# Kernel tuning notes

Measured on AMD Instinct MI355X. Metric: run time of the kernel, lower is better.

The kernel has to match this reference:

```python
import jax, jax.numpy as jnp
import numpy as np

HEADS = 16
DIM_HEAD = 64


def setup_inputs() -> dict:
    key = jax.random.key(0)
    k1, k2, k3 = jax.random.split(key, 3)
    b, n, dim = 8, 4096, 1024
    inner = HEADS * DIM_HEAD  # 1024
    x = jax.random.normal(k1, (b, n, dim), dtype=jnp.float32)
    # torch Linear stored transposed; here W_qkv is [in, out] so y = x @ W_qkv
    W_qkv = jax.random.normal(k2, (dim, 4 * inner), dtype=jnp.float32) * (dim ** -0.5)
    W_out = jax.random.normal(k3, (inner, dim), dtype=jnp.float32) * (inner ** -0.5)
    b_out = jnp.zeros((dim,), dtype=jnp.float32)
    return {"x": x, "W_qkv": W_qkv, "W_out": W_out, "b_out": b_out}


def reference(x, W_qkv, W_out, b_out):
    b, n, dim = x.shape
    h, d = HEADS, DIM_HEAD
    scale = d ** -0.5
    qkv = x @ W_qkv  # [b, n, 4*h*d]
    q, k, v, v2 = jnp.split(qkv, 4, axis=-1)
    # rearrange 'b n (h d) -> b h n d'
    to_heads = lambda t: t.reshape(b, n, h, d).transpose(0, 2, 1, 3)
    q, k, v, v2 = map(to_heads, (q, k, v, v2))
    # channel-wise attention: dots = q^T @ k over the sequence axis -> [b,h,d,d]
    dots = jnp.einsum('bhnd,bhne->bhde', q, k) * scale
    attn = jax.nn.softmax(dots, axis=-1)
    # v^T @ v2 -> [b,h,d,d]
    vv = jnp.einsum('bhnd,bhne->bhde', v, v2)
    out = jnp.einsum('bhde,bhef->bhdf', attn, vv)  # [b,h,d,d]
    # rearrange 'b h n d -> b n (h d)' with n == dim_head here
    out = out.transpose(0, 2, 1, 3).reshape(b, d, h * d)  # [b, dim_head, inner]
    return out @ W_out + b_out  # [b, dim_head, dim]
```

## Files before the change

kernel.cpp:

```cpp
#include <hip/hip_runtime.h>
#include <hip/hip_bf16.h>
#include <stdint.h>

typedef _Float16 f16;
typedef _Float16 f16x8 __attribute__((ext_vector_type(8)));
typedef float f32x4 __attribute__((ext_vector_type(4)));

#define AS1 __attribute__((address_space(1)))
#define AS3 __attribute__((address_space(3)))

__global__ __launch_bounds__(256) void tr_cvt_all(
    const float* __restrict__ x, const float* __restrict__ Wqkv,
    const float* __restrict__ Wout,
    f16* __restrict__ xT, f16* __restrict__ WqkvT, f16* __restrict__ WoutT)
{
    __shared__ float tile[64][65];
    const int id = blockIdx.x;
    const int t = threadIdx.x;

    const float* src; f16* dst; int R, C, c0, r0;
    if (id < 8192) {
        const int b = id >> 10, rem = id & 1023;
        src = x + (size_t)b * 4096 * 1024;
        dst = xT + (size_t)b * 4096 * 1024;
        R = 4096; C = 1024;
        c0 = (rem & 15) * 64; r0 = (rem >> 4) * 64;
    } else if (id < 9216) {
        const int rem = id - 8192;
        src = Wqkv; dst = WqkvT;
        R = 1024; C = 4096;
        c0 = (rem & 63) * 64; r0 = (rem >> 6) * 64;
    } else {
        const int rem = id - 9216;
        src = Wout; dst = WoutT;
        R = 1024; C = 1024;
        c0 = (rem & 15) * 64; r0 = (rem >> 4) * 64;
    }

    {
        const int cc = (t & 15) * 4;
        const int rr = t >> 4;
#pragma unroll
        for (int p = 0; p < 4; ++p) {
            const int r = rr + p * 16;
            const float4 v = *(const float4*)(src + (size_t)(r0 + r) * C + c0 + cc);
            tile[r][cc + 0] = v.x; tile[r][cc + 1] = v.y;
            tile[r][cc + 2] = v.z; tile[r][cc + 3] = v.w;
        }
    }
    __syncthreads();
    {
        const int rq = (t & 15) * 4;
        const int cp = t >> 4;
#pragma unroll
        for (int p = 0; p < 4; ++p) {
            const int c = cp + p * 16;
            ushort4 o;
            f16 h0 = (f16)tile[rq + 0][c];
            f16 h1 = (f16)tile[rq + 1][c];
            f16 h2 = (f16)tile[rq + 2][c];
            f16 h3 = (f16)tile[rq + 3][c];
            o.x = __builtin_bit_cast(unsigned short, h0);
            o.y = __builtin_bit_cast(unsigned short, h1);
            o.z = __builtin_bit_cast(unsigned short, h2);
            o.w = __builtin_bit_cast(unsigned short, h3);
            *(ushort4*)(dst + (size_t)(c0 + c) * R + r0 + rq) = o;
        }
    }
}

__device__ __forceinline__ void stage256(
    const f16* __restrict__ src, int ld, char* ldsbase, int tid)
{
    const int lane = tid & 63;
    const int gch = ((lane & 7) ^ (lane >> 3)) * 8;
    const int rowl = tid >> 3;
    const int wbase = (tid >> 3) & ~7;
#pragma unroll
    for (int p = 0; p < 4; ++p) {
        const f16* s = src + (size_t)(p * 64 + rowl) * ld + gch;
        __builtin_amdgcn_global_load_lds(
            (const AS1 uint32_t*)s,
            (AS3 uint32_t*)(ldsbase + (p * 64 + wbase) * 128), 16, 0, 0);
    }
}

__device__ __forceinline__ void gemm256_core(
    const f16* __restrict__ A, const f16* __restrict__ Bt,
    int lda, int ldb, int nsteps,
    f16* As, f16* Bs, f32x4 (&acc)[8][4], int tid)
{
    const int lane = tid & 63, w = tid >> 6;
    const int wr = w >> 2, wc = w & 3;
    const int cl = lane & 15, kg = lane >> 4, b7 = lane & 7;

    stage256(A, lda, (char*)As, tid);
    stage256(Bt, ldb, (char*)Bs, tid);

#pragma unroll 1
    for (int t = 0; t < nsteps; ++t) {
        const int cur = t & 1;
        if (t + 1 < nsteps) {
            const int k0 = (t + 1) * 64;
            stage256(A + k0, lda, (char*)As + (cur ^ 1) * 32768, tid);
            stage256(Bt + k0, ldb, (char*)Bs + (cur ^ 1) * 32768, tid);
            asm volatile("s_waitcnt vmcnt(8)" ::: "memory");
        } else {
            asm volatile("s_waitcnt vmcnt(0)" ::: "memory");
        }
        __builtin_amdgcn_s_barrier();
        const f16* Ab = As + cur * 16384;
        const f16* Bb = Bs + cur * 16384;
#pragma unroll
        for (int kk = 0; kk < 2; ++kk) {
            const int ch = (kk * 4 + kg) ^ b7;
            f16x8 af[8], bf[4];
#pragma unroll
            for (int i = 0; i < 8; ++i)
                af[i] = *(const f16x8*)&Ab[(wr * 128 + i * 16 + cl) * 64 + ch * 8];
#pragma unroll
            for (int j = 0; j < 4; ++j)
                bf[j] = *(const f16x8*)&Bb[(wc * 64 + j * 16 + cl) * 64 + ch * 8];
#pragma unroll
            for (int i = 0; i < 8; ++i)
#pragma unroll
                for (int j = 0; j < 4; ++j)
                    acc[i][j] = __builtin_amdgcn_mfma_f32_16x16x32_f16(af[i], bf[j], acc[i][j], 0, 0, 0);
        }
        __builtin_amdgcn_s_barrier();
    }
}

__global__ __launch_bounds__(512, 2) void gemm_syk256(
    const f16* __restrict__ xT, f16* __restrict__ Gp)
{
    __shared__ f16 As[2 * 256 * 64];
    __shared__ f16 Bs[2 * 256 * 64];
    const int orig = blockIdx.x;
    const int l = (orig & 7) * 32 + (orig >> 3);
    const int tile = l & 15, b = (l >> 4) & 7, s = l >> 7;
    const int ti = tile >> 2, tj = tile & 3;

    const f16* base = xT + (size_t)b * (1024 * 4096) + (size_t)s * 2048;
    const f16* A  = base + (size_t)ti * 256 * 4096;
    const f16* Bt = base + (size_t)tj * 256 * 4096;

    f32x4 acc[8][4];
#pragma unroll
    for (int i = 0; i < 8; ++i)
#pragma unroll
        for (int j = 0; j < 4; ++j) acc[i][j] = f32x4{0.f, 0.f, 0.f, 0.f};

    gemm256_core(A, Bt, 4096, 4096, 32, As, Bs, acc, threadIdx.x);

    f16* out = Gp + ((size_t)s * 8 + b) * 1048576;
    const int lane = threadIdx.x & 63, w = threadIdx.x >> 6;
    const int wr = w >> 2, wc = w & 3;
    const int cl = lane & 15, rg = lane >> 4;
#pragma unroll
    for (int i = 0; i < 8; ++i)
#pragma unroll
        for (int j = 0; j < 4; ++j)
#pragma unroll
            for (int q = 0; q < 4; ++q) {
                const int row = ti * 256 + wr * 128 + i * 16 + rg * 4 + q;
                const int col = tj * 256 + wc * 64 + j * 16 + cl;
                out[(size_t)row * 1024 + col] = (f16)acc[i][j][q];
            }
}

__global__ __launch_bounds__(256) void reduce_sum(
    const f16* __restrict__ Gp, f16* __restrict__ G)
{
    const size_t i = ((size_t)blockIdx.x * 256 + threadIdx.x) * 8;
    const f16x8 a = *(const f16x8*)(Gp + i);
    const f16x8 c = *(const f16x8*)(Gp + 8388608 + i);
    f16x8 o;
#pragma unroll
    for (int j = 0; j < 8; ++j) o[j] = (f16)((float)a[j] + (float)c[j]);
    *(f16x8*)(G + i) = o;
}

__global__ __launch_bounds__(512, 2) void gemm_qv256(
    const f16* __restrict__ WqkvT, const f16* __restrict__ G,
    f16* __restrict__ UW2)
{
    __shared__ f16 As[2 * 256 * 64];
    __shared__ f16 Bs[2 * 256 * 64];
    const int orig = blockIdx.x;
    const int l = (orig & 7) * 32 + (orig >> 3);
    const int bx = l & 3, by = (l >> 2) & 7, b = l >> 5;
    const int arow = (by < 4) ? by * 256 : 2048 + (by - 4) * 256;

    const f16* A  = WqkvT + (size_t)arow * 1024;
    const f16* Bt = G + (size_t)b * 1048576 + (size_t)bx * 256 * 1024;

    f32x4 acc[8][4];
#pragma unroll
    for (int i = 0; i < 8; ++i)
#pragma unroll
        for (int j = 0; j < 4; ++j) acc[i][j] = f32x4{0.f, 0.f, 0.f, 0.f};

    gemm256_core(A, Bt, 1024, 1024, 16, As, Bs, acc, threadIdx.x);

    f16* C = UW2 + (size_t)b * 2097152;
    const int lane = threadIdx.x & 63, w = threadIdx.x >> 6;
    const int wr = w >> 2, wc = w & 3;
    const int cl = lane & 15, rg = lane >> 4;
#pragma unroll
    for (int i = 0; i < 8; ++i)
#pragma unroll
        for (int j = 0; j < 4; ++j) {
            const int cc = bx * 256 + wc * 64 + j * 16 + cl;
#pragma unroll
            for (int q = 0; q < 4; ++q) {
                const int rr = by * 256 + wr * 128 + i * 16 + rg * 4 + q;
                C[(size_t)rr * 1024 + cc] = (f16)acc[i][j][q];
            }
        }
}

__device__ __forceinline__ void gemm_body(
    const f16* __restrict__ A, const f16* __restrict__ Bt,
    int lda, int ldb, int K, f16* As, f16* Bs,
    f32x4 (&acc)[4][4], int tid)
{
    const int lane = tid & 63, w = tid >> 6;
    const int wr = w >> 1, wc = w & 1;
    const int lrow = lane >> 3;
    const int lcol = (lane & 7) * 8;
    for (int k0 = 0; k0 < K; k0 += 64) {
#pragma unroll
        for (int p = 0; p < 4; ++p) {
            const f16* sa = A + (size_t)(p * 32 + w * 8 + lrow) * lda + k0 + lcol;
            __builtin_amdgcn_global_load_lds(
                (const AS1 uint32_t*)sa,
                (AS3 uint32_t*)((char*)As + p * 4096 + w * 1024), 16, 0, 0);
            const f16* sb = Bt + (size_t)(p * 32 + w * 8 + lrow) * ldb + k0 + lcol;
            __builtin_amdgcn_global_load_lds(
                (const AS1 uint32_t*)sb,
                (AS3 uint32_t*)((char*)Bs + p * 4096 + w * 1024), 16, 0, 0);
        }
        __syncthreads();
#pragma unroll
        for (int kk = 0; kk < 2; ++kk) {
            f16x8 af[4], bfr[4];
#pragma unroll
            for (int i = 0; i < 4; ++i)
                af[i] = *(const f16x8*)&As[(wr * 64 + i * 16 + (lane & 15)) * 64 + kk * 32 + (lane >> 4) * 8];
#pragma unroll
            for (int j = 0; j < 4; ++j)
                bfr[j] = *(const f16x8*)&Bs[(wc * 64 + j * 16 + (lane & 15)) * 64 + kk * 32 + (lane >> 4) * 8];
#pragma unroll
            for (int i = 0; i < 4; ++i)
#pragma unroll
                for (int j = 0; j < 4; ++j)
                    acc[i][j] = __builtin_amdgcn_mfma_f32_16x16x32_f16(af[i], bfr[j], acc[i][j], 0, 0, 0);
        }
        __syncthreads();
    }
}

__global__ __launch_bounds__(256) void gemm_out(
    const f16* __restrict__ A, const f16* __restrict__ Bt,
    const float* __restrict__ bias, float* __restrict__ Cout)
{
    __shared__ f16 As[128 * 64];
    __shared__ f16 Bs[128 * 64];
    const int tn0 = blockIdx.x * 128;
    const int tm0 = blockIdx.y * 128;
    f32x4 acc[4][4];
#pragma unroll
    for (int i = 0; i < 4; ++i)
#pragma unroll
        for (int j = 0; j < 4; ++j) acc[i][j] = f32x4{0.f, 0.f, 0.f, 0.f};

    gemm_body(A + (size_t)tm0 * 1024, Bt + (size_t)tn0 * 1024,
              1024, 1024, 1024, As, Bs, acc, threadIdx.x);

    const int lane = threadIdx.x & 63, w = threadIdx.x >> 6;
    const int wr = w >> 1, wc = w & 1;
    const int cl = lane & 15, rg = lane >> 4;
#pragma unroll
    for (int i = 0; i < 4; ++i)
#pragma unroll
        for (int j = 0; j < 4; ++j) {
            const int cc = tn0 + wc * 64 + j * 16 + cl;
            const float bv = bias[cc];
#pragma unroll
            for (int q = 0; q < 4; ++q) {
                const int rr = tm0 + wr * 64 + i * 16 + rg * 4 + q;
                Cout[(size_t)rr * 1024 + cc] = acc[i][j][q] + bv;
            }
        }
}

__global__ __launch_bounds__(512) void attn_small(
    const f16* __restrict__ UW2, const f16* __restrict__ WqkvT,
    f16* __restrict__ O)
{
    __shared__ float dots[64][66];
    __shared__ float vv[64][66];
    const int h = blockIdx.x, b = blockIdx.y;
    const int tid = threadIdx.x, lane = tid & 63, w = tid >> 6;
    const int isVV = w >> 2;
    const int kq = w & 3;

    const f16* Arows = UW2 + (size_t)b * (2048 * 1024)
                           + (size_t)isVV * (1024 * 1024) + (size_t)h * 64 * 1024;
    const f16* Brows = WqkvT + (size_t)(isVV ? 3072 : 1024) * 1024 + (size_t)h * 64 * 1024;

    f32x4 acc[4][4];
#pragma unroll
    for (int i = 0; i < 4; ++i)
#pragma unroll
        for (int j = 0; j < 4; ++j) acc[i][j] = f32x4{0.f, 0.f, 0.f, 0.f};

    const int cl = lane & 15, kg = lane >> 4;
    for (int ks = 0; ks < 8; ++ks) {
        const int k0 = kq * 256 + ks * 32 + kg * 8;
        f16x8 af[4], bfr[4];
#pragma unroll
        for (int i = 0; i < 4; ++i)
            af[i] = *(const f16x8*)(Arows + (size_t)(i * 16 + cl) * 1024 + k0);
#pragma unroll
        for (int j = 0; j < 4; ++j)
            bfr[j] = *(const f16x8*)(Brows + (size_t)(j * 16 + cl) * 1024 + k0);
#pragma unroll
        for (int i = 0; i < 4; ++i)
#pragma unroll
            for (int j = 0; j < 4; ++j)
                acc[i][j] = __builtin_amdgcn_mfma_f32_16x16x32_f16(af[i], bfr[j], acc[i][j], 0, 0, 0);
    }

    float (*dst)[66] = isVV ? vv : dots;
#pragma unroll
    for (int r = 0; r < 4; ++r) {
        if (kq == r) {
            if (r == 0) {
#pragma unroll
                for (int i = 0; i < 4; ++i)
#pragma unroll
                    for (int j = 0; j < 4; ++j)
#pragma unroll
                        for (int q = 0; q < 4; ++q)
                            dst[i * 16 + kg * 4 + q][j * 16 + cl] = acc[i][j][q];
            } else {
#pragma unroll
                for (int i = 0; i < 4; ++i)
#pragma unroll
                    for (int j = 0; j < 4; ++j)
#pragma unroll
                        for (int q = 0; q < 4; ++q)
                            dst[i * 16 + kg * 4 + q][j * 16 + cl] += acc[i][j][q];
            }
        }
        __syncthreads();
    }

    if (tid < 64) {
        const int r = tid;
        float mx = -1e30f;
        for (int e = 0; e < 64; ++e) {
            const float v = dots[r][e] * 0.125f;
            dots[r][e] = v;
            mx = fmaxf(mx, v);
        }
        float s = 0.f;
        for (int e = 0; e < 64; ++e) {
            const float v = __expf(dots[r][e] - mx);
            dots[r][e] = v;
            s += v;
        }
        const float inv = 1.f / s;
        for (int e = 0; e < 64; ++e) dots[r][e] *= inv;
    }
    __syncthreads();

    {
        const int r = tid >> 3, f0 = (tid & 7) * 8;
        float o[8];
#pragma unroll
        for (int i = 0; i < 8; ++i) o[i] = 0.f;
        for (int e = 0; e < 64; ++e) {
            const float a = dots[r][e];
#pragma unroll
            for (int i = 0; i < 8; ++i) o[i] += a * vv[e][f0 + i];
        }
        f16* Od = O + (size_t)b * 64 * 1024 + (size_t)r * 1024 + h * 64 + f0;
#pragma unroll
        for (int i = 0; i < 8; ++i) Od[i] = (f16)o[i];
    }
}

extern "C" void kernel_launch(void* const* d_in, const int* in_sizes, int n_in,
                              void* d_out, int out_size, void* d_ws, size_t ws_size,
                              hipStream_t stream)
{
    const float* x    = (const float*)d_in[0];
    const float* Wqkv = (const float*)d_in[1];
    const float* Wout = (const float*)d_in[2];
    const float* bout = (const float*)d_in[3];

    char* ws = (char*)d_ws;
    f16* xT    = (f16*)(ws + 0);
    f16* WqkvT = (f16*)(ws + 67108864);
    f16* WoutT = (f16*)(ws + 75497472);
    f16* G     = (f16*)(ws + 77594624);
    f16* Gp    = (f16*)(ws + 94371840);
    f16* UW2   = (f16*)(ws + 94371840);
    f16* O     = (f16*)(ws + 127926272);

    tr_cvt_all<<<9472, 256, 0, stream>>>(x, Wqkv, Wout, xT, WqkvT, WoutT);

    gemm_syk256<<<256, 512, 0, stream>>>(xT, Gp);
    reduce_sum<<<4096, 256, 0, stream>>>(Gp, G);
    gemm_qv256<<<256, 512, 0, stream>>>(WqkvT, G, UW2);
    attn_small<<<dim3(16, 8), 512, 0, stream>>>(UW2, WqkvT, O);
    gemm_out<<<dim3(8, 4), 256, 0, stream>>>(O, WoutT, bout, (float*)d_out);
}
```

Before: 197.2 us.

## Exploit Gram-matrix symmetry: compute upper-triangle tiles only and mirror in reduce

The X^T X Gram GEMM now computes only the 10 upper-triangular 256x256 tiles per batch instead of all 16. The K dimension is rebalanced into three splits (22/21/21 steps) so that 240 blocks fit one wave. A new reduce kernel sums the three partials, writes each tile, and writes the transposed copy through shared memory for off-diagonal tiles. This cuts matrix-multiply work by roughly a third, at the cost of an extra partial, a transpose with possible LDS bank conflicts, and a large shared-memory footprint in the reduce.

Result: faster. 180.1 us (-8.7%).

```diff
diff --git a/kernel.cpp b/kernel.cpp
--- a/kernel.cpp
+++ b/kernel.cpp
@@ -137,11 +137,17 @@
     __shared__ f16 As[2 * 256 * 64];
     __shared__ f16 Bs[2 * 256 * 64];
     const int orig = blockIdx.x;
-    const int l = (orig & 7) * 32 + (orig >> 3);
-    const int tile = l & 15, b = (l >> 4) & 7, s = l >> 7;
-    const int ti = tile >> 2, tj = tile & 3;
-
-    const f16* base = xT + (size_t)b * (1024 * 4096) + (size_t)s * 2048;
+    const int l = (orig & 7) * 30 + (orig >> 3);
+    const int u = l % 10;
+    const int b = (l / 10) & 7;
+    const int s = l / 80;
+    int ti = 0, rem = u;
+    while (rem >= 4 - ti) { rem -= 4 - ti; ++ti; }
+    const int tj = ti + rem;
+    const int koff = (s == 0) ? 0 : (1408 + (s - 1) * 1344);
+    const int nst  = (s == 0) ? 22 : 21;
+
+    const f16* base = xT + (size_t)b * (1024 * 4096) + koff;
     const f16* A  = base + (size_t)ti * 256 * 4096;
     const f16* Bt = base + (size_t)tj * 256 * 4096;
 
@@ -151,9 +157,9 @@
 #pragma unroll
         for (int j = 0; j < 4; ++j) acc[i][j] = f32x4{0.f, 0.f, 0.f, 0.f};
 
-    gemm256_core(A, Bt, 4096, 4096, 32, As, Bs, acc, threadIdx.x);
-
-    f16* out = Gp + ((size_t)s * 8 + b) * 1048576;
+    gemm256_core(A, Bt, 4096, 4096, nst, As, Bs, acc, threadIdx.x);
+
+    f16* out = Gp + ((size_t)s * 80 + b * 10 + u) * 65536;
     const int lane = threadIdx.x & 63, w = threadIdx.x >> 6;
     const int wr = w >> 2, wc = w & 3;
     const int cl = lane & 15, rg = lane >> 4;
@@ -163,22 +169,62 @@
         for (int j = 0; j < 4; ++j)
 #pragma unroll
             for (int q = 0; q < 4; ++q) {
-                const int row = ti * 256 + wr * 128 + i * 16 + rg * 4 + q;
-                const int col = tj * 256 + wc * 64 + j * 16 + cl;
-                out[(size_t)row * 1024 + col] = (f16)acc[i][j][q];
+                const int row = wr * 128 + i * 16 + rg * 4 + q;
+                const int col = wc * 64 + j * 16 + cl;
+                out[row * 256 + col] = (f16)acc[i][j][q];
             }
 }
 
-__global__ __launch_bounds__(256) void reduce_sum(
+__global__ __launch_bounds__(256) void reduce_mirror(
     const f16* __restrict__ Gp, f16* __restrict__ G)
 {
-    const size_t i = ((size_t)blockIdx.x * 256 + threadIdx.x) * 8;
-    const f16x8 a = *(const f16x8*)(Gp + i);
-    const f16x8 c = *(const f16x8*)(Gp + 8388608 + i);
-    f16x8 o;
-#pragma unroll
-    for (int j = 0; j < 8; ++j) o[j] = (f16)((float)a[j] + (float)c[j]);
-    *(f16x8*)(G + i) = o;
+    __shared__ float tile[128][129];
+    const int q = blockIdx.x, u = blockIdx.y, b = blockIdx.z;
+    int ti = 0, rem = u;
+    while (rem >= 4 - ti) { rem -= 4 - ti; ++ti; }
+    const int tj = ti + rem;
+    const int qr = q >> 1, qc = q & 1;
+    const size_t tb = ((size_t)b * 10 + u) * 65536;
+    const size_t sstride = (size_t)80 * 65536;
+    f16* Gb = G + (size_t)b * 1048576;
+    const int t = threadIdx.x;
+
+#pragma unroll
+    for (int i = 0; i < 8; ++i) {
+        const int e = (i * 256 + t) * 8;
+        const int r = e >> 7, c = e & 127;
+        const size_t src = tb + (size_t)(qr * 128 + r) * 256 + qc * 128 + c;
+        float sum[8];
+#pragma unroll
+        for (int j = 0; j < 8; ++j) sum[j] = 0.f;
+#pragma unroll
+        for (int sp = 0; sp < 3; ++sp) {
+            const f16x8 v = *(const f16x8*)(Gp + sp * sstride + src);
+#pragma unroll
+            for (int j = 0; j < 8; ++j) sum[j] += (float)v[j];
+        }
+        f16x8 o;
+#pragma unroll
+        for (int j = 0; j < 8; ++j) {
+            o[j] = (f16)sum[j];
+            tile[r][c + j] = sum[j];
+        }
+        *(f16x8*)(Gb + (size_t)(ti * 256 + qr * 128 + r) * 1024
+                     + tj * 256 + qc * 128 + c) = o;
+    }
+    if (ti != tj) {
+        __syncthreads();
+#pragma unroll
+        for (int i = 0; i < 8; ++i) {
+            const int e = (i * 256 + t) * 8;
+            const int R = e >> 7, C = e & 127;
+            f16x8 o;
+#pragma unroll
+            for (int j = 0; j < 8; ++j) o[j] = (f16)tile[C + j][R];
+            *(f16x8*)(Gb + (size_t)(tj * 256 + qc * 128 + R) * 1024
+                         + ti * 256 + qr * 128 + C) = o;
+        }
+    }
 }
 
 __global__ __launch_bounds__(512, 2) void gemm_qv256(
@@ -413,8 +459,8 @@
 
     tr_cvt_all<<<9472, 256, 0, stream>>>(x, Wqkv, Wout, xT, WqkvT, WoutT);
 
-    gemm_syk256<<<256, 512, 0, stream>>>(xT, Gp);
-    reduce_sum<<<4096, 256, 0, stream>>>(Gp, G);
+    gemm_syk256<<<240, 512, 0, stream>>>(xT, Gp);
+    reduce_mirror<<<dim3(4, 10, 8), 256, 0, stream>>>(Gp, G);
     gemm_qv256<<<256, 512, 0, stream>>>(WqkvT, G, UW2);
     attn_small<<<dim3(16, 8), 512, 0, stream>>>(UW2, WqkvT, O);
     gemm_out<<<dim3(8, 4), 256, 0, stream>>>(O, WoutT, bout, (float*)d_out);
```
